# Performance work log

Measured on AMD Instinct MI355X. Metric: run time of the kernel, lower is better.

Reference implementation:

```python
import jax, jax.numpy as jnp
import numpy as np

G, N, H = 64, 512, 64          # graphs, nodes/graph, hidden
NT = G * N                     # total nodes
DEG = 32
ET = NT * DEG                  # total edges
KP = int(np.ceil(0.7 * N))     # TopKPooling keep per graph (359)
NP2 = G * KP                   # nodes after pooling
F_IN, NC, NA = 128, 2, 6
seg = jax.ops.segment_sum


def graph_norm(h, batch, num_g, w, b, ms, eps=1e-5):
    cnt = seg(jnp.ones((h.shape[0], 1), h.dtype), batch, num_segments=num_g)
    mean = seg(h, batch, num_segments=num_g) / cnt
    hc = h - ms * mean[batch]
    var = seg(hc * hc, batch, num_segments=num_g) / cnt
    return w * hc / jnp.sqrt(var[batch] + eps) + b


def sage(h, src, tgt, valid, Ws, Wn, b, n_nodes):
    # PyG SAGEConv (mean aggr): out_i = x_i@Ws + mean_{j->i} x_j @ Wn + b
    msg = h[src] * valid[:, None]
    agg = seg(msg, tgt, num_segments=n_nodes)
    deg = seg(valid, tgt, num_segments=n_nodes)
    return h @ Ws + (agg / jnp.maximum(deg, 1.0)[:, None]) @ Wn + b


def setup_inputs() -> dict:
    key = jax.random.key(0)
    ks = jax.random.split(key, 20)
    offs = (jnp.arange(G) * N)[:, None]
    src = (jax.random.randint(ks[0], (G, N * DEG), 0, N) + offs).reshape(-1)
    tgt = (jax.random.randint(ks[1], (G, N * DEG), 0, N) + offs).reshape(-1)
    edge_index = jnp.stack([src, tgt])  # within-graph edges

    def lin(k, fi, fo):
        return jax.random.normal(k, (fi, fo), jnp.float32) / np.sqrt(fi)

    return {
        "x": jax.random.normal(ks[2], (NT, F_IN), jnp.float32),
        "edge_index": edge_index,
        "edge_attr": jax.random.uniform(ks[3], (ET,), jnp.float32),
        "coords": jax.random.normal(ks[4], (NT, 3), jnp.float32),
        "anatomical_class": jax.random.randint(ks[5], (NT,), 0, NA),
        "Bk_table": jax.random.normal(ks[6], (NA, H * H), jnp.float32) * 0.05,
        "pos_W": lin(ks[7], 3, H), "pos_b": jnp.zeros((H,), jnp.float32),
        "W1_self": lin(ks[8], F_IN, H), "W1_neigh": lin(ks[9], F_IN, H),
        "b1": jnp.zeros((H,), jnp.float32),
        "gn1_w": jnp.ones((H,), jnp.float32), "gn1_b": jnp.zeros((H,), jnp.float32),
        "gn1_ms": jnp.ones((H,), jnp.float32),
        "pool_p": jax.random.normal(ks[10], (H,), jnp.float32),
        "W2_self": lin(ks[11], H, H), "W2_neigh": lin(ks[12], H, H),
        "b2": jnp.zeros((H,), jnp.float32),
        "gn2_w": jnp.ones((H,), jnp.float32), "gn2_b": jnp.zeros((H,), jnp.float32),
        "gn2_ms": jnp.ones((H,), jnp.float32),
        "lin1_W": lin(ks[13], 3 * H, H), "lin1_b": jnp.zeros((H,), jnp.float32),
        "lin2_W": lin(ks[14], H, NC), "lin2_b": jnp.zeros((NC,), jnp.float32),
    }


def reference(x, edge_index, edge_attr, coords, anatomical_class, Bk_table,
              pos_W, pos_b, W1_self, W1_neigh, b1, gn1_w, gn1_b, gn1_ms,
              pool_p, W2_self, W2_neigh, b2, gn2_w, gn2_b, gn2_ms,
              lin1_W, lin1_b, lin2_W, lin2_b):
    row, col = edge_index[0], edge_index[1]
    batch = jnp.repeat(jnp.arange(G), N)
    # ---- stage 1: anatomical propagation kernel ----
    e = coords @ pos_W + pos_b                                 # [NT, H]
    Ae = seg(edge_attr[:, None] * e[col], row, num_segments=NT)  # SpMM adj @ e
    Bk = Bk_table[anatomical_class].reshape(NT, H, H)
    delta = jnp.einsum('nd,nhd->nh', Ae, Bk)                   # bmm(Ae, Bk^T)
    ones_e = jnp.ones((ET,), x.dtype)
    h = sage(x, row, col, ones_e, W1_self, W1_neigh, b1, NT)
    h = jax.nn.elu(graph_norm(h, batch, G, gn1_w, gn1_b, gn1_ms))
    h = h + delta
    h = jnp.einsum('nij,nj->ni', Bk + delta[:, :, None], h)    # propagate_message
    # ---- TopK pooling (equal-sized graphs) ----
    score = (h @ pool_p) / jnp.linalg.norm(pool_p)
    vals, idx = jax.lax.top_k(score.reshape(G, N), KP)
    perm = (idx + (jnp.arange(G) * N)[:, None]).reshape(-1)    # [NP2]
    h = h[perm] * jnp.tanh(vals).reshape(-1)[:, None]
    batch2 = jnp.repeat(jnp.arange(G), KP)
    node_map = jnp.full((NT,), -1, jnp.int32).at[perm].set(jnp.arange(NP2, dtype=jnp.int32))
    s2, t2 = node_map[row], node_map[col]
    valid = ((s2 >= 0) & (t2 >= 0)).astype(h.dtype)            # masked edge filter
    s2 = jnp.where(s2 >= 0, s2, 0)
    t2 = jnp.where(t2 >= 0, t2, 0)
    # ---- stage 2 ----
    e2 = coords[perm] @ pos_W + pos_b
    Bk2 = Bk_table[anatomical_class[perm]].reshape(NP2, H, H)
    Ae2 = seg(valid[:, None] * e2[t2], s2, num_segments=NP2)   # edge_attr = ones
    delta2 = jnp.einsum('nd,nhd->nh', Ae2, Bk2)
    h = h + delta2
    h = jnp.einsum('nij,nj->ni', Bk2 + delta2[:, :, None], h)
    h = sage(h, s2, t2, valid, W2_self, W2_neigh, b2, NP2)
    h = jax.nn.elu(graph_norm(h, batch2, G, gn2_w, gn2_b, gn2_ms))
    # ---- readout ----
    cnt = seg(jnp.ones((NP2, 1), h.dtype), batch2, num_segments=G)
    hsum = seg(h, batch2, num_segments=G)
    g = jnp.concatenate([hsum / cnt,
                         jax.ops.segment_max(h, batch2, num_segments=G),
                         hsum], axis=1)
    g = jax.nn.relu(g @ lin1_W + lin1_b)
    return jax.nn.log_softmax(g @ lin2_W + lin2_b, axis=1)
```

## Files before the change

### kernel.cpp

```cpp
#include <hip/hip_runtime.h>
#include <math.h>

#define G_    64
#define N_    512
#define H_    64
#define NT_   32768
#define ET_   1048576
#define EPG_  16384
#define KP_   359
#define NP2_  22976
#define FIN_  128
#define ESL_  2048
#define BPB_  (EPG_/ESL_)

__global__ void k_bkT(const float* __restrict__ Bk, float* __restrict__ BkT) {
    int idx = blockIdx.x * 256 + threadIdx.x;
    int c = idx >> 12, r = idx & 4095;
    int h = r >> 6, d = r & 63;
    BkT[c * 4096 + d * 64 + h] = Bk[c * 4096 + h * 64 + d];
}

__global__ void k_pre(const float* __restrict__ Bk, const float* __restrict__ posW,
                      const float* __restrict__ posb, float* __restrict__ PT) {
    int c = blockIdx.x;
    int t = threadIdx.x;
    int i = t >> 6, h = t & 63;
    const float* B = Bk + c * 4096 + h * 64;
    float acc = 0.f;
    for (int d = 0; d < 64; d++) {
        float vd = (i < 3) ? posW[i*64 + d] : posb[d];
        acc += B[d] * vd;
    }
    PT[c*256 + i*64 + h] = acc;
}

__global__ __launch_bounds__(256)
void k_hist(const int* __restrict__ row, const int* __restrict__ col,
            int* __restrict__ histR, int* __restrict__ histC) {
    __shared__ int hr[N_], hc[N_];
    int b = blockIdx.x, g = b >> 3, s = b & (BPB_ - 1);
    int t = threadIdx.x;
    for (int i = t; i < N_; i += 256) { hr[i] = 0; hc[i] = 0; }
    __syncthreads();
    int ebase = g * EPG_ + s * ESL_;
    for (int i = t; i < ESL_; i += 256) {
        atomicAdd(&hr[row[ebase + i] & (N_ - 1)], 1);
        atomicAdd(&hc[col[ebase + i] & (N_ - 1)], 1);
    }
    __syncthreads();
    int nbase = g * N_;
    for (int i = t; i < N_; i += 256) {
        if (hr[i]) atomicAdd(&histR[nbase + i], hr[i]);
        if (hc[i]) atomicAdd(&histC[nbase + i], hc[i]);
    }
}

__global__ __launch_bounds__(256)
void k_scan(int* __restrict__ histR, int* __restrict__ histC,
            int* __restrict__ rowptr, int* __restrict__ colptr,
            float* __restrict__ deg) {
    __shared__ int hr[N_], hc[N_];
    int g = blockIdx.x, t = threadIdx.x;
    int nbase = g * N_;
    for (int i = t; i < N_; i += 256) {
        hr[i] = histR[nbase + i];
        int c = histC[nbase + i];
        hc[i] = c;
        deg[nbase + i] = (float)c;
    }
    __syncthreads();
    int wave = t >> 6, lane = t & 63;
    if (wave < 2) {
        int* h = wave ? hc : hr;
        int base8 = lane * 8;
        int loc[8];
        int tot = 0;
        #pragma unroll
        for (int i = 0; i < 8; i++) { int v = h[base8 + i]; loc[i] = tot; tot += v; }
        int pref = tot;
        for (int off = 1; off < 64; off <<= 1) {
            int u = __shfl_up(pref, off);
            if (lane >= off) pref += u;
        }
        pref -= tot;
        #pragma unroll
        for (int i = 0; i < 8; i++) h[base8 + i] = pref + loc[i];
    }
    __syncthreads();
    int ebase = g * EPG_;
    for (int i = t; i < N_; i += 256) {
        int rp = ebase + hr[i], cp = ebase + hc[i];
        rowptr[nbase + i] = rp;  histR[nbase + i] = rp;
        colptr[nbase + i] = cp;  histC[nbase + i] = cp;
    }
    if (g == 0 && t == 0) { rowptr[NT_] = ET_; colptr[NT_] = ET_; }
}

__global__ __launch_bounds__(256)
void k_scatter(const int* __restrict__ row, const int* __restrict__ col,
               const float* __restrict__ ea,
               int* __restrict__ cursR, int* __restrict__ cursC,
               int2* __restrict__ rowcsr, int* __restrict__ colcsr) {
    int b = blockIdx.x, g = b >> 3, s = b & (BPB_ - 1);
    int t = threadIdx.x;
    int ebase = g * EPG_ + s * ESL_;
    for (int i = t; i < ESL_; i += 256) {
        int rg = row[ebase + i], cg = col[ebase + i];
        float w = ea[ebase + i];
        int pr = atomicAdd(&cursR[rg], 1);
        rowcsr[pr] = make_int2(cg, __float_as_int(w));
        int pc = atomicAdd(&cursC[cg], 1);
        colcsr[pc] = rg;
    }
}

__global__ __launch_bounds__(256)
void k_gemm_dual(const float* __restrict__ in, int K,
                 const float* __restrict__ Wa, const float* __restrict__ Wb,
                 const float* __restrict__ bias, const int* __restrict__ permA,
                 float* __restrict__ outA, float* __restrict__ outB) {
    __shared__ float inT[32 * FIN_];
    int row0 = blockIdx.x * 32;
    int t = threadIdx.x;
    for (int idx = t; idx < 32 * K; idx += 256) inT[idx] = in[row0 * K + idx];
    __syncthreads();
    int c = t & 63, rb = t >> 6;
    const float* ip = inT + (rb * 8) * K;
    float aA[8] = {0,0,0,0,0,0,0,0};
    float aB[8] = {0,0,0,0,0,0,0,0};
    for (int k = 0; k < K; k += 4) {
        float wa0 = Wa[(k+0)*64 + c], wa1 = Wa[(k+1)*64 + c];
        float wa2 = Wa[(k+2)*64 + c], wa3 = Wa[(k+3)*64 + c];
        float wb0 = Wb[(k+0)*64 + c], wb1 = Wb[(k+1)*64 + c];
        float wb2 = Wb[(k+2)*64 + c], wb3 = Wb[(k+3)*64 + c];
        #pragma unroll
        for (int r = 0; r < 8; r++) {
            float4 xv = *(const float4*)&ip[r*K + k];
            aA[r] += xv.x*wa0; aB[r] += xv.x*wb0;
            aA[r] += xv.y*wa1; aB[r] += xv.y*wb1;
            aA[r] += xv.z*wa2; aB[r] += xv.z*wb2;
            aA[r] += xv.w*wa3; aB[r] += xv.w*wb3;
        }
    }
    float bv = bias[c];
    #pragma unroll
    for (int r = 0; r < 8; r++) {
        int node = row0 + rb*8 + r;
        int rowA = permA ? permA[node] : node;
        outA[rowA*64 + c] = aA[r];
        outB[node*64 + c] = aB[r] + bv;
    }
}

__global__ __launch_bounds__(256)
void k_nsum1(const int* __restrict__ rowptr, const int2* __restrict__ rcsr,
             const float* __restrict__ coords, float4* __restrict__ nsum) {
    int node = blockIdx.x * 4 + (threadIdx.x >> 6);
    int lane = threadIdx.x & 63;
    int start = rowptr[node], end = rowptr[node + 1];
    float sx = 0.f, sy = 0.f, sz = 0.f, sw = 0.f;
    for (int k = start + lane; k < end; k += 64) {
        int2 ent = rcsr[k];
        int c = ent.x;
        float w = __int_as_float(ent.y);
        sx += w * coords[c*3+0];
        sy += w * coords[c*3+1];
        sz += w * coords[c*3+2];
        sw += w;
    }
    #pragma unroll
    for (int off = 32; off; off >>= 1) {
        sx += __shfl_xor(sx, off); sy += __shfl_xor(sy, off);
        sz += __shfl_xor(sz, off); sw += __shfl_xor(sw, off);
    }
    if (lane == 0) nsum[node] = make_float4(sx, sy, sz, sw);
}

__global__ __launch_bounds__(256)
void k_gagg(const int* __restrict__ colptr, const int* __restrict__ ccsr,
            const float* __restrict__ y, float* __restrict__ agg) {
    int node = blockIdx.x * 4 + (threadIdx.x >> 6);
    int lane = threadIdx.x & 63;
    int start = colptr[node], end = colptr[node + 1];
    float acc = 0.f;
    #pragma unroll 4
    for (int k = start; k < end; k++) {
        int r = ccsr[k];
        acc += y[r*64 + lane];
    }
    agg[node*64 + lane] = acc;
}

__global__ __launch_bounds__(256)
void k_gnstat(const float* __restrict__ hs, const float* __restrict__ agg,
              const float* __restrict__ deg, float* __restrict__ partial,
              int NPG, int CH, int npc) {
    __shared__ float r1[256], r2[256];
    int b = blockIdx.x;
    int g = b / CH, chunk = b % CH;
    int t = threadIdx.x, c = t & 63, grp = t >> 6;
    int n0 = chunk * npc;
    int nend = min(n0 + npc, NPG);
    float s1 = 0.f, s2 = 0.f;
    for (int n = n0 + grp; n < nend; n += 4) {
        int node = g * NPG + n;
        float v = hs[node*64 + c] + agg[node*64 + c] / fmaxf(deg[node], 1.f);
        s1 += v; s2 += v * v;
    }
    r1[t] = s1; r2[t] = s2;
    __syncthreads();
    if (grp == 0) {
        partial[b*128 + c]      = r1[c] + r1[64+c] + r1[128+c] + r1[192+c];
        partial[b*128 + 64 + c] = r2[c] + r2[64+c] + r2[128+c] + r2[192+c];
    }
}

__global__ void k_gnfin(const float* __restrict__ partial, const float* __restrict__ ms,
                        int CH, int NPG,
                        float* __restrict__ mval, float* __restrict__ istdv) {
    int g = blockIdx.x, t = threadIdx.x;
    float s1 = 0.f, s2 = 0.f;
    for (int i = 0; i < CH; i++) {
        s1 += partial[(g*CH + i)*128 + t];
        s2 += partial[(g*CH + i)*128 + 64 + t];
    }
    float m = s1 / (float)NPG, q = s2 / (float)NPG, msv = ms[t];
    float var = q - msv * m * m * (2.f - msv);
    mval[g*64 + t]  = msv * m;
    istdv[g*64 + t] = rsqrtf(var + 1e-5f);
}

__global__ __launch_bounds__(256)
void k_gnprop(const float* __restrict__ hself, const float* __restrict__ agg,
              const float* __restrict__ deg,
              const float* __restrict__ mval, const float* __restrict__ istdv,
              const float* __restrict__ w, const float* __restrict__ b,
              const float4* __restrict__ nsum, const int* __restrict__ cls,
              const float* __restrict__ PT, const float* __restrict__ BkT,
              float* __restrict__ out) {
    __shared__ float hT[256];
    int t = threadIdx.x;
    int node = blockIdx.x * 4 + (t >> 6);
    int lane = t & 63;
    int g = node >> 9;
    float4 s4 = nsum[node];
    int c = cls[node];
    const float* P = PT + c * 256;
    float d = s4.x*P[lane] + s4.y*P[64+lane] + s4.z*P[128+lane] + s4.w*P[192+lane];
    float v = hself[node*64 + lane] + agg[node*64 + lane] / fmaxf(deg[node], 1.f);
    v = w[lane] * (v - mval[g*64 + lane]) * istdv[g*64 + lane] + b[lane];
    v = v > 0.f ? v : expm1f(v);
    v += d;
    hT[t] = v;
    __syncthreads();
    float ssum = v;
    #pragma unroll
    for (int off = 32; off; off >>= 1) ssum += __shfl_xor(ssum, off);
    const float* B  = BkT + c * 4096;
    const float* hv = hT + (t & ~63);
    float acc = 0.f;
    #pragma unroll 8
    for (int j = 0; j < 64; j++) acc += B[j*64 + lane] * hv[j];
    out[node*64 + lane] = acc + d * ssum;
}

__global__ void k_topk(const float* __restrict__ hp, const float* __restrict__ p,
                       const int* __restrict__ cls,
                       int* __restrict__ perm, float* __restrict__ tanhv,
                       int* __restrict__ node_map, int* __restrict__ class2) {
    __shared__ float key[N_];
    __shared__ int   idxS[N_];
    __shared__ float pS[64];
    __shared__ float nrm;
    int g = blockIdx.x, t = threadIdx.x;
    if (t < 64) pS[t] = p[t];
    __syncthreads();
    if (t == 0) {
        float s = 0.f;
        for (int i = 0; i < 64; i++) s += pS[i] * pS[i];
        nrm = sqrtf(s);
    }
    __syncthreads();
    {
        float acc = 0.f;
        const float* hv = hp + (size_t)(g*N_ + t) * 64;
        for (int cdx = 0; cdx < 64; cdx++) acc += hv[cdx] * pS[cdx];
        key[t]  = acc / nrm;
        idxS[t] = t;
    }
    __syncthreads();
    for (int k = 2; k <= N_; k <<= 1) {
        for (int j = k >> 1; j > 0; j >>= 1) {
            int i = t, ixj = i ^ j;
            if (ixj > i) {
                float ki = key[i], kj = key[ixj];
                int   ii = idxS[i], ij = idxS[ixj];
                bool before = (ki > kj) || (ki == kj && ii < ij);
                bool dir = ((i & k) == 0);
                if (dir ? !before : before) {
                    key[i] = kj; key[ixj] = ki;
                    idxS[i] = ij; idxS[ixj] = ii;
                }
            }
            __syncthreads();
        }
    }
    if (t < KP_) {
        int orig  = idxS[t];
        int gnode = g * N_ + orig;
        int pj    = g * KP_ + t;
        perm[pj]     = gnode;
        tanhv[pj]    = tanhf(key[t]);
        node_map[gnode] = pj;
        class2[pj]   = cls[gnode];
    }
}

__global__ __launch_bounds__(256)
void k_s2pre(const int* __restrict__ rowptr, const int2* __restrict__ rcsr,
             const int* __restrict__ colptr, const int* __restrict__ ccsr,
             const int* __restrict__ perm, const int* __restrict__ nmap,
             const float* __restrict__ coords,
             float4* __restrict__ nsum2, float* __restrict__ deg2) {
    int j = blockIdx.x * 4 + (threadIdx.x >> 6);
    int lane = threadIdx.x & 63;
    int orig = perm[j];
    int start = rowptr[orig], end = rowptr[orig + 1];
    float sx = 0.f, sy = 0.f, sz = 0.f, sw = 0.f;
    for (int k = start + lane; k < end; k += 64) {
        int c = rcsr[k].x;
        if (nmap[c] >= 0) {
            sx += coords[c*3+0]; sy += coords[c*3+1]; sz += coords[c*3+2];
            sw += 1.f;
        }
    }
    int cs = colptr[orig], ce = colptr[orig + 1];
    float dg = 0.f;
    for (int k = cs + lane; k < ce; k += 64) {
        if (nmap[ccsr[k]] >= 0) dg += 1.f;
    }
    #pragma unroll
    for (int off = 32; off; off >>= 1) {
        sx += __shfl_xor(sx, off); sy += __shfl_xor(sy, off);
        sz += __shfl_xor(sz, off); sw += __shfl_xor(sw, off);
        dg += __shfl_xor(dg, off);
    }
    if (lane == 0) { nsum2[j] = make_float4(sx, sy, sz, sw); deg2[j] = dg; }
}

__global__ __launch_bounds__(256)
void k_prop2v(const float* __restrict__ hp, const int* __restrict__ perm,
              const float* __restrict__ tanhv,
              const float4* __restrict__ nsum2, const int* __restrict__ cls2,
              const float* __restrict__ PT, const float* __restrict__ BkT,
              float* __restrict__ out) {
    __shared__ float hT[256];
    int t = threadIdx.x;
    int j = blockIdx.x * 4 + (t >> 6);
    int lane = t & 63;
    int orig = perm[j];
    float tv = tanhv[j];
    float4 s4 = nsum2[j];
    int c = cls2[j];
    const float* P = PT + c * 256;
    float d = s4.x*P[lane] + s4.y*P[64+lane] + s4.z*P[128+lane] + s4.w*P[192+lane];
    float v = hp[orig*64 + lane] * tv + d;
    hT[t] = v;
    __syncthreads();
    float ssum = v;
    #pragma unroll
    for (int off = 32; off; off >>= 1) ssum += __shfl_xor(ssum, off);
    const float* B  = BkT + c * 4096;
    const float* hv = hT + (t & ~63);
    float acc = 0.f;
    #pragma unroll 8
    for (int jj = 0; jj < 64; jj++) acc += B[jj*64 + lane] * hv[jj];
    out[j*64 + lane] = acc + d * ssum;
}

__global__ __launch_bounds__(256)
void k_gagg2(const int* __restrict__ colptr, const int* __restrict__ ccsr,
             const int* __restrict__ perm, const float* __restrict__ y2full,
             float* __restrict__ agg2) {
    int j = blockIdx.x * 4 + (threadIdx.x >> 6);
    int lane = threadIdx.x & 63;
    int orig = perm[j];
    int start = colptr[orig], end = colptr[orig + 1];
    float acc = 0.f;
    #pragma unroll 4
    for (int k = start; k < end; k++) {
        int r = ccsr[k];
        acc += y2full[r*64 + lane];
    }
    agg2[j*64 + lane] = acc;
}

__global__ __launch_bounds__(256)
void k_gnrd(const float* __restrict__ hs, const float* __restrict__ agg,
            const float* __restrict__ deg2,
            const float* __restrict__ mval, const float* __restrict__ istdv,
            const float* __restrict__ w, const float* __restrict__ b,
            float* __restrict__ part, int CH, int npc) {
    __shared__ float r1[256], r2[256];
    int blk = blockIdx.x;
    int g = blk / CH, chunk = blk % CH;
    int t = threadIdx.x, c = t & 63, grp = t >> 6;
    int n0 = chunk * npc, nend = min(n0 + npc, KP_);
    float mv = mval[g*64 + c], is = istdv[g*64 + c], wv = w[c], bv = b[c];
    float s = 0.f, m = -1e30f;
    for (int n = n0 + grp; n < nend; n += 4) {
        int node = g * KP_ + n;
        float v = hs[node*64 + c] + agg[node*64 + c] / fmaxf(deg2[node], 1.f);
        v = wv * (v - mv) * is + bv;
        v = v > 0.f ? v : expm1f(v);
        s += v; m = fmaxf(m, v);
    }
    r1[t] = s; r2[t] = m;
    __syncthreads();
    if (grp == 0) {
        part[blk*128 + c]      = r1[c] + r1[64+c] + r1[128+c] + r1[192+c];
        part[blk*128 + 64 + c] = fmaxf(fmaxf(r2[c], r2[64+c]), fmaxf(r2[128+c], r2[192+c]));
    }
}

__global__ void k_rfin(const float* __restrict__ part, int CH,
                       const float* __restrict__ l1W, const float* __restrict__ l1b,
                       const float* __restrict__ l2W, const float* __restrict__ l2b,
                       float* __restrict__ out) {
    __shared__ float gv[192], rS[64];
    int g = blockIdx.x, t = threadIdx.x;
    float s = 0.f, m = -1e30f;
    for (int i = 0; i < CH; i++) {
        s += part[(g*CH + i)*128 + t];
        m = fmaxf(m, part[(g*CH + i)*128 + 64 + t]);
    }
    gv[t] = s / (float)KP_;
    gv[64 + t] = m;
    gv[128 + t] = s;
    __syncthreads();
    float acc = l1b[t];
    for (int k = 0; k < 192; k++) acc += gv[k] * l1W[k*64 + t];
    rS[t] = fmaxf(acc, 0.f);
    __syncthreads();
    if (t == 0) {
        float l0 = l2b[0], l1v = l2b[1];
        for (int hh = 0; hh < 64; hh++) { l0 += rS[hh]*l2W[hh*2+0]; l1v += rS[hh]*l2W[hh*2+1]; }
        float mx  = fmaxf(l0, l1v);
        float lse = mx + logf(expf(l0 - mx) + expf(l1v - mx));
        out[g*2 + 0] = l0  - lse;
        out[g*2 + 1] = l1v - lse;
    }
}

extern "C" void kernel_launch(void* const* d_in, const int* in_sizes, int n_in,
                              void* d_out, int out_size, void* d_ws, size_t ws_size,
                              hipStream_t stream) {
    const float* x      = (const float*)d_in[0];
    const int*   eidx   = (const int*)  d_in[1];
    const float* eattr  = (const float*)d_in[2];
    const float* coords = (const float*)d_in[3];
    const int*   acls   = (const int*)  d_in[4];
    const float* BkTab  = (const float*)d_in[5];
    const float* posW   = (const float*)d_in[6];
    const float* posb   = (const float*)d_in[7];
    const float* W1s    = (const float*)d_in[8];
    const float* W1n    = (const float*)d_in[9];
    const float* b1     = (const float*)d_in[10];
    const float* gn1w   = (const float*)d_in[11];
    const float* gn1b   = (const float*)d_in[12];
    const float* gn1ms  = (const float*)d_in[13];
    const float* poolp  = (const float*)d_in[14];
    const float* W2s    = (const float*)d_in[15];
    const float* W2n    = (const float*)d_in[16];
    const float* b2     = (const float*)d_in[17];
    const float* gn2w   = (const float*)d_in[18];
    const float* gn2b   = (const float*)d_in[19];
    const float* gn2ms  = (const float*)d_in[20];
    const float* l1W    = (const float*)d_in[21];
    const float* l1b    = (const float*)d_in[22];
    const float* l2W    = (const float*)d_in[23];
    const float* l2b    = (const float*)d_in[24];

    const int* row  = eidx;
    const int* colp = eidx + ET_;

    float* W = (float*)d_ws;
    const size_t NTH = (size_t)NT_ * 64;
    float* b0    = W;
    float* b1buf = W + 1*NTH;
    float* b2buf = W + 2*NTH;
    float* b3buf = W + 3*NTH;
    float* p = W + 4*NTH;
    int2*  rowcsr = (int2*)p;        p += 2*(size_t)ET_;
    int*   colcsr = (int*)p;         p += ET_;
    int*   rowptr = (int*)p;         p += NT_ + 8;
    int*   colptr = (int*)p;         p += NT_ + 8;
    int*   histR  = (int*)p;         p += NT_;
    int*   histC  = (int*)p;         p += NT_;
    float* deg    = p;               p += NT_;
    float* deg2   = p;               p += NP2_;
    float* tanhv  = p;               p += NP2_;
    int*   perm   = (int*)p;         p += NP2_;
    int*   nmap   = (int*)p;         p += NT_;
    int*   cls2   = (int*)p;         p += NP2_;
    float* BkT    = p;               p += 6 * 4096;
    float* PT     = p;               p += 6 * 256;
    float* meanv  = p;               p += G_ * 64;
    float* istdv  = p;               p += G_ * 64;
    float* partial= (float*)histR;
    float4* nsum  = (float4*)b3buf;
    float4* nsum2 = (float4*)b3buf;

    hipMemsetAsync(histR, 0, 2 * NT_ * sizeof(int), stream);
    hipMemsetAsync(nmap, 0xFF, NT_ * sizeof(int), stream);
    k_bkT      <<<96,       256, 0, stream>>>(BkTab, BkT);
    k_pre      <<<6,        256, 0, stream>>>(BkTab, posW, posb, PT);
    k_hist     <<<G_*BPB_,  256, 0, stream>>>(row, colp, histR, histC);
    k_scan     <<<G_,       256, 0, stream>>>(histR, histC, rowptr, colptr, deg);
    k_scatter  <<<G_*BPB_,  256, 0, stream>>>(row, colp, eattr, histR, histC,
                                              rowcsr, colcsr);

    k_gemm_dual<<<NT_/32,  256, 0, stream>>>(x, FIN_, W1n, W1s, b1, nullptr,
                                             b0 , b1buf );
    k_nsum1    <<<NT_/4,   256, 0, stream>>>(rowptr, rowcsr, coords, nsum);
    k_gagg     <<<NT_/4,   256, 0, stream>>>(colptr, colcsr, b0 , b2buf );
    k_gnstat   <<<G_*8,    256, 0, stream>>>(b1buf , b2buf , deg,
                                             partial, N_, 8, 64);
    k_gnfin    <<<G_,      64,  0, stream>>>(partial, gn1ms, 8, N_, meanv, istdv);
    k_gnprop   <<<NT_/4,   256, 0, stream>>>(b1buf , b2buf , deg,
                                             meanv, istdv, gn1w, gn1b,
                                             nsum, acls, PT, BkT,
                                             b1buf );
    k_topk     <<<G_,      512, 0, stream>>>(b1buf , poolp, acls,
                                             perm, tanhv, nmap, cls2);

    k_s2pre    <<<NP2_/4,  256, 0, stream>>>(rowptr, rowcsr, colptr, colcsr,
                                             perm, nmap, coords, nsum2, deg2);
    k_prop2v   <<<NP2_/4,  256, 0, stream>>>(b1buf , perm, tanhv,
                                             nsum2, cls2, PT, BkT, b2buf );
    hipMemsetAsync(b0, 0, NTH * sizeof(float), stream);
    k_gemm_dual<<<NP2_/32, 256, 0, stream>>>(b2buf , 64, W2n, W2s, b2, perm,
                                             b0 , b3buf );
    k_gagg2    <<<NP2_/4,  256, 0, stream>>>(colptr, colcsr, perm, b0 ,
                                             b1buf );
    k_gnstat   <<<G_*6,    256, 0, stream>>>(b3buf , b1buf , deg2,
                                             partial, KP_, 6, 60);
    k_gnfin    <<<G_,      64,  0, stream>>>(partial, gn2ms, 6, KP_, meanv, istdv);
    k_gnrd     <<<G_*6,    256, 0, stream>>>(b3buf , b1buf , deg2,
                                             meanv, istdv, gn2w, gn2b,
                                             partial, 6, 60);
    k_rfin     <<<G_,      64,  0, stream>>>(partial, 6, l1W, l1b, l2W, l2b,
                                             (float*)d_out);
}
```

Measured before the change: 404.4 us.

## Fuse prep, edge-gather and stage-2 kernels; rebuild CSR scatter with shared-memory cursors

Merges the Bk transpose and P precompute into one launch, folds the nmap reset into the scan kernel, fuses the coordinate-sum and neighbour-aggregate kernels for stage 1, and fuses the stage-2 pre-pass with the propagation kernel. The CSR scatter now uses 1024-thread blocks, each owning a quarter of a graph's nodes, with cursors held in LDS instead of global atomics. This cuts launch count, removes intermediate round trips, and replaces contended global atomics, at the cost of each scatter block reading the whole graph's edge list four times. It also bumps gather unroll from 4 to 8.

```diff
diff --git a/kernel.cpp b/kernel.cpp
--- a/kernel.cpp
+++ b/kernel.cpp
@@ -13,25 +13,26 @@
 #define ESL_  2048
 #define BPB_  (EPG_/ESL_)
 
-__global__ void k_bkT(const float* __restrict__ Bk, float* __restrict__ BkT) {
-    int idx = blockIdx.x * 256 + threadIdx.x;
-    int c = idx >> 12, r = idx & 4095;
-    int h = r >> 6, d = r & 63;
-    BkT[c * 4096 + d * 64 + h] = Bk[c * 4096 + h * 64 + d];
-}
-
-__global__ void k_pre(const float* __restrict__ Bk, const float* __restrict__ posW,
-                      const float* __restrict__ posb, float* __restrict__ PT) {
-    int c = blockIdx.x;
-    int t = threadIdx.x;
-    int i = t >> 6, h = t & 63;
-    const float* B = Bk + c * 4096 + h * 64;
-    float acc = 0.f;
-    for (int d = 0; d < 64; d++) {
-        float vd = (i < 3) ? posW[i*64 + d] : posb[d];
-        acc += B[d] * vd;
-    }
-    PT[c*256 + i*64 + h] = acc;
+__global__ void k_prep(const float* __restrict__ Bk, const float* __restrict__ posW,
+                       const float* __restrict__ posb,
+                       float* __restrict__ BkT, float* __restrict__ PT) {
+    int b = blockIdx.x, t = threadIdx.x;
+    if (b < 96) {
+        int idx = b * 256 + t;
+        int c = idx >> 12, r = idx & 4095;
+        int h = r >> 6, d = r & 63;
+        BkT[c * 4096 + d * 64 + h] = Bk[c * 4096 + h * 64 + d];
+    } else {
+        int c = b - 96;
+        int i = t >> 6, h = t & 63;
+        const float* B = Bk + c * 4096 + h * 64;
+        float acc = 0.f;
+        for (int d = 0; d < 64; d++) {
+            float vd = (i < 3) ? posW[i*64 + d] : posb[d];
+            acc += B[d] * vd;
+        }
+        PT[c*256 + i*64 + h] = acc;
+    }
 }
 
 __global__ __launch_bounds__(256)
@@ -56,9 +57,9 @@
 }
 
 __global__ __launch_bounds__(256)
-void k_scan(int* __restrict__ histR, int* __restrict__ histC,
+void k_scan(const int* __restrict__ histR, const int* __restrict__ histC,
             int* __restrict__ rowptr, int* __restrict__ colptr,
-            float* __restrict__ deg) {
+            float* __restrict__ deg, int* __restrict__ nmap) {
     __shared__ int hr[N_], hc[N_];
     int g = blockIdx.x, t = threadIdx.x;
     int nbase = g * N_;
@@ -67,6 +68,7 @@
         int c = histC[nbase + i];
         hc[i] = c;
         deg[nbase + i] = (float)c;
+        nmap[nbase + i] = -1;
     }
     __syncthreads();
     int wave = t >> 6, lane = t & 63;
@@ -89,28 +91,38 @@
     __syncthreads();
     int ebase = g * EPG_;
     for (int i = t; i < N_; i += 256) {
-        int rp = ebase + hr[i], cp = ebase + hc[i];
-        rowptr[nbase + i] = rp;  histR[nbase + i] = rp;
-        colptr[nbase + i] = cp;  histC[nbase + i] = cp;
+        rowptr[nbase + i] = ebase + hr[i];
+        colptr[nbase + i] = ebase + hc[i];
     }
     if (g == 0 && t == 0) { rowptr[NT_] = ET_; colptr[NT_] = ET_; }
 }
 
-__global__ __launch_bounds__(256)
-void k_scatter(const int* __restrict__ row, const int* __restrict__ col,
-               const float* __restrict__ ea,
-               int* __restrict__ cursR, int* __restrict__ cursC,
-               int2* __restrict__ rowcsr, int* __restrict__ colcsr) {
-    int b = blockIdx.x, g = b >> 3, s = b & (BPB_ - 1);
+__global__ __launch_bounds__(1024)
+void k_scat(const int* __restrict__ row, const int* __restrict__ col,
+            const float* __restrict__ ea,
+            const int* __restrict__ rowptr, const int* __restrict__ colptr,
+            int2* __restrict__ rowcsr, int* __restrict__ colcsr) {
+    __shared__ int curR[128], curC[128];
+    int g = blockIdx.x >> 2, q = blockIdx.x & 3;
     int t = threadIdx.x;
-    int ebase = g * EPG_ + s * ESL_;
-    for (int i = t; i < ESL_; i += 256) {
-        int rg = row[ebase + i], cg = col[ebase + i];
-        float w = ea[ebase + i];
-        int pr = atomicAdd(&cursR[rg], 1);
-        rowcsr[pr] = make_int2(cg, __float_as_int(w));
-        int pc = atomicAdd(&cursC[cg], 1);
-        colcsr[pc] = rg;
+    int lo = q * 128;
+    int nbase = g * N_ + lo;
+    if (t < 128) { curR[t] = rowptr[nbase + t]; curC[t] = colptr[nbase + t]; }
+    __syncthreads();
+    int ebase = g * EPG_;
+    for (int i = t; i < EPG_; i += 1024) {
+        int rg = row[ebase + i];
+        int cg = col[ebase + i];
+        int rl = (rg & (N_ - 1)) - lo;
+        if ((unsigned)rl < 128u) {
+            int pr = atomicAdd(&curR[rl], 1);
+            rowcsr[pr] = make_int2(cg, __float_as_int(ea[ebase + i]));
+        }
+        int cl = (cg & (N_ - 1)) - lo;
+        if ((unsigned)cl < 128u) {
+            int pc = atomicAdd(&curC[cl], 1);
+            colcsr[pc] = rg;
+        }
     }
 }
 
@@ -153,13 +165,15 @@
 }
 
 __global__ __launch_bounds__(256)
-void k_nsum1(const int* __restrict__ rowptr, const int2* __restrict__ rcsr,
-             const float* __restrict__ coords, float4* __restrict__ nsum) {
+void k_edge1f(const int* __restrict__ rowptr, const int2* __restrict__ rcsr,
+              const int* __restrict__ colptr, const int* __restrict__ ccsr,
+              const float* __restrict__ coords, const float* __restrict__ y,
+              float4* __restrict__ nsum, float* __restrict__ agg) {
     int node = blockIdx.x * 4 + (threadIdx.x >> 6);
     int lane = threadIdx.x & 63;
-    int start = rowptr[node], end = rowptr[node + 1];
+    int rs = rowptr[node], re = rowptr[node + 1];
     float sx = 0.f, sy = 0.f, sz = 0.f, sw = 0.f;
-    for (int k = start + lane; k < end; k += 64) {
+    for (int k = rs + lane; k < re; k += 64) {
         int2 ent = rcsr[k];
         int c = ent.x;
         float w = __int_as_float(ent.y);
@@ -174,17 +188,10 @@
         sz += __shfl_xor(sz, off); sw += __shfl_xor(sw, off);
     }
     if (lane == 0) nsum[node] = make_float4(sx, sy, sz, sw);
-}
-
-__global__ __launch_bounds__(256)
-void k_gagg(const int* __restrict__ colptr, const int* __restrict__ ccsr,
-            const float* __restrict__ y, float* __restrict__ agg) {
-    int node = blockIdx.x * 4 + (threadIdx.x >> 6);
-    int lane = threadIdx.x & 63;
-    int start = colptr[node], end = colptr[node + 1];
+    int cs = colptr[node], ce = colptr[node + 1];
     float acc = 0.f;
-    #pragma unroll 4
-    for (int k = start; k < end; k++) {
+    #pragma unroll 8
+    for (int k = cs; k < ce; k++) {
         int r = ccsr[k];
         acc += y[r*64 + lane];
     }
@@ -317,17 +324,22 @@
 }
 
 __global__ __launch_bounds__(256)
-void k_s2pre(const int* __restrict__ rowptr, const int2* __restrict__ rcsr,
-             const int* __restrict__ colptr, const int* __restrict__ ccsr,
-             const int* __restrict__ perm, const int* __restrict__ nmap,
-             const float* __restrict__ coords,
-             float4* __restrict__ nsum2, float* __restrict__ deg2) {
-    int j = blockIdx.x * 4 + (threadIdx.x >> 6);
-    int lane = threadIdx.x & 63;
+void k_s2prop(const int* __restrict__ rowptr, const int2* __restrict__ rcsr,
+              const int* __restrict__ colptr, const int* __restrict__ ccsr,
+              const int* __restrict__ perm, const int* __restrict__ nmap,
+              const float* __restrict__ coords,
+              const float* __restrict__ hp, const float* __restrict__ tanhv,
+              const int* __restrict__ cls2,
+              const float* __restrict__ PT, const float* __restrict__ BkT,
+              float* __restrict__ out, float* __restrict__ deg2) {
+    __shared__ float hT[256];
+    int t = threadIdx.x;
+    int j = blockIdx.x * 4 + (t >> 6);
+    int lane = t & 63;
     int orig = perm[j];
-    int start = rowptr[orig], end = rowptr[orig + 1];
+    int rs = rowptr[orig], re = rowptr[orig + 1];
     float sx = 0.f, sy = 0.f, sz = 0.f, sw = 0.f;
-    for (int k = start + lane; k < end; k += 64) {
+    for (int k = rs + lane; k < re; k += 64) {
         int c = rcsr[k].x;
         if (nmap[c] >= 0) {
             sx += coords[c*3+0]; sy += coords[c*3+1]; sz += coords[c*3+2];
@@ -345,26 +357,11 @@
         sz += __shfl_xor(sz, off); sw += __shfl_xor(sw, off);
         dg += __shfl_xor(dg, off);
     }
-    if (lane == 0) { nsum2[j] = make_float4(sx, sy, sz, sw); deg2[j] = dg; }
-}
-
-__global__ __launch_bounds__(256)
-void k_prop2v(const float* __restrict__ hp, const int* __restrict__ perm,
-              const float* __restrict__ tanhv,
-              const float4* __restrict__ nsum2, const int* __restrict__ cls2,
-              const float* __restrict__ PT, const float* __restrict__ BkT,
-              float* __restrict__ out) {
-    __shared__ float hT[256];
-    int t = threadIdx.x;
-    int j = blockIdx.x * 4 + (t >> 6);
-    int lane = t & 63;
-    int orig = perm[j];
-    float tv = tanhv[j];
-    float4 s4 = nsum2[j];
+    if (lane == 0) deg2[j] = dg;
     int c = cls2[j];
     const float* P = PT + c * 256;
-    float d = s4.x*P[lane] + s4.y*P[64+lane] + s4.z*P[128+lane] + s4.w*P[192+lane];
-    float v = hp[orig*64 + lane] * tv + d;
+    float d = sx*P[lane] + sy*P[64+lane] + sz*P[128+lane] + sw*P[192+lane];
+    float v = hp[orig*64 + lane] * tanhv[j] + d;
     hT[t] = v;
     __syncthreads();
     float ssum = v;
@@ -387,7 +384,7 @@
     int orig = perm[j];
     int start = colptr[orig], end = colptr[orig + 1];
     float acc = 0.f;
-    #pragma unroll 4
+    #pragma unroll 8
     for (int k = start; k < end; k++) {
         int r = ccsr[k];
         acc += y2full[r*64 + lane];
@@ -507,23 +504,20 @@
     float* PT     = p;               p += 6 * 256;
     float* meanv  = p;               p += G_ * 64;
     float* istdv  = p;               p += G_ * 64;
-    float* partial= (float*)histR;
+    float* partial= p;               p += (size_t)G_ * 8 * 128;
     float4* nsum  = (float4*)b3buf;
-    float4* nsum2 = (float4*)b3buf;
 
     hipMemsetAsync(histR, 0, 2 * NT_ * sizeof(int), stream);
-    hipMemsetAsync(nmap, 0xFF, NT_ * sizeof(int), stream);
-    k_bkT      <<<96,       256, 0, stream>>>(BkTab, BkT);
-    k_pre      <<<6,        256, 0, stream>>>(BkTab, posW, posb, PT);
-    k_hist     <<<G_*BPB_,  256, 0, stream>>>(row, colp, histR, histC);
-    k_scan     <<<G_,       256, 0, stream>>>(histR, histC, rowptr, colptr, deg);
-    k_scatter  <<<G_*BPB_,  256, 0, stream>>>(row, colp, eattr, histR, histC,
+    k_prep     <<<102,     256,  0, stream>>>(BkTab, posW, posb, BkT, PT);
+    k_hist     <<<G_*BPB_, 256,  0, stream>>>(row, colp, histR, histC);
+    k_scan     <<<G_,      256,  0, stream>>>(histR, histC, rowptr, colptr, deg, nmap);
+    k_scat     <<<G_*4,    1024, 0, stream>>>(row, colp, eattr, rowptr, colptr,
                                               rowcsr, colcsr);
 
     k_gemm_dual<<<NT_/32,  256, 0, stream>>>(x, FIN_, W1n, W1s, b1, nullptr,
                                              b0 , b1buf );
-    k_nsum1    <<<NT_/4,   256, 0, stream>>>(rowptr, rowcsr, coords, nsum);
-    k_gagg     <<<NT_/4,   256, 0, stream>>>(colptr, colcsr, b0 , b2buf );
+    k_edge1f   <<<NT_/4,   256, 0, stream>>>(rowptr, rowcsr, colptr, colcsr,
+                                             coords, b0 , nsum, b2buf );
     k_gnstat   <<<G_*8,    256, 0, stream>>>(b1buf , b2buf , deg,
                                              partial, N_, 8, 64);
     k_gnfin    <<<G_,      64,  0, stream>>>(partial, gn1ms, 8, N_, meanv, istdv);
@@ -534,10 +528,10 @@
     k_topk     <<<G_,      512, 0, stream>>>(b1buf , poolp, acls,
                                              perm, tanhv, nmap, cls2);
 
-    k_s2pre    <<<NP2_/4,  256, 0, stream>>>(rowptr, rowcsr, colptr, colcsr,
-                                             perm, nmap, coords, nsum2, deg2);
-    k_prop2v   <<<NP2_/4,  256, 0, stream>>>(b1buf , perm, tanhv,
-                                             nsum2, cls2, PT, BkT, b2buf );
+    k_s2prop   <<<NP2_/4,  256, 0, stream>>>(rowptr, rowcsr, colptr, colcsr,
+                                             perm, nmap, coords,
+                                             b1buf , tanhv, cls2, PT, BkT,
+                                             b2buf , deg2);
     hipMemsetAsync(b0, 0, NTH * sizeof(float), stream);
     k_gemm_dual<<<NP2_/32, 256, 0, stream>>>(b2buf , 64, W2n, W2s, b2, perm,
                                              b0 , b3buf );
```

After: 343.8 us. 1.18x faster.
